# Optimization experiments

Measured on AMD Instinct MI355X. Metric: run time of the kernel, lower is better.

Reference implementation:

```python
import jax, jax.numpy as jnp
import numpy as np

N = 21  # nodes per graph (20 laser sectors + 1 robot node)
MAX_RANGE = 10.0
_bound = np.linspace(-np.pi / 2 - 0.03, np.pi / 2, 21, dtype=np.float32)[:-1]
_angles = _bound + np.float32(np.pi / 20)
ANGLE_FEAT = jnp.asarray(np.stack([np.sin(_angles), np.cos(_angles)], 1), dtype=jnp.float32)  # [20,2]


def _build_nodes(state24):
    # state24: [B,24] -> node features [B,21,7]
    B = state24.shape[0]
    laser = state24[:, :20, None] / MAX_RANGE                       # [B,20,1]
    angle = jnp.broadcast_to(ANGLE_FEAT[None], (B, 20, 2))          # [B,20,2]
    sector = jnp.concatenate([laser, angle, jnp.zeros((B, 20, 4), state24.dtype)], -1)  # [B,20,7]
    robot = jnp.concatenate([jnp.zeros((B, 1, 3), state24.dtype), state24[:, None, 20:]], -1)  # [B,1,7]
    return jnp.concatenate([sector, robot], axis=1)                 # [B,21,7]


def _gatv2(x, Wl, Wr, att, bias, heads, dim):
    # GATv2 over a fully-connected graph with self-loops (dense all-pairs).
    # e_ij = att . leaky_relu(Wl x_j + Wr x_i); alpha = softmax_j; out_i = sum_j alpha_ij (Wl x_j)
    B = x.shape[0]
    gl = (x @ Wl).reshape(B, N, heads, dim)  # source transform [B,j,H,D]
    gr = (x @ Wr).reshape(B, N, heads, dim)  # target transform [B,i,H,D]
    s = jax.nn.leaky_relu(gl[:, None] + gr[:, :, None], negative_slope=0.2)  # [B,i,j,H,D]
    e = jnp.einsum('bijhd,hd->bijh', s, att)                                  # [B,i,j,H]
    alpha = jax.nn.softmax(e, axis=2)                                          # softmax over sources j
    out = jnp.einsum('bijh,bjhd->bihd', alpha, gl).reshape(B, N, heads * dim)
    return out + bias


def setup_inputs() -> dict:
    key = jax.random.key(0)
    ks = jax.random.split(key, 16)
    r = lambda k, shape, s: (jax.random.normal(k, shape, dtype=jnp.float32) * s)
    B = 1024
    return {
        'state24': jax.random.normal(ks[0], (B, 24), dtype=jnp.float32),
        'Wl1': r(ks[1], (7, 256), 0.3), 'Wr1': r(ks[2], (7, 256), 0.3),
        'att1': r(ks[3], (4, 64), 0.1), 'b1': r(ks[4], (256,), 0.02),
        'Wl2': r(ks[5], (256, 64), 0.06), 'Wr2': r(ks[6], (256, 64), 0.06),
        'att2': r(ks[7], (1, 64), 0.1), 'b2': r(ks[8], (64,), 0.02),
        'fc1_w': r(ks[9], (64, 256), 0.12), 'fc1_b': r(ks[10], (256,), 0.02),
        'fc2_w': r(ks[11], (256, 256), 0.06), 'fc2_b': r(ks[12], (256,), 0.02),
        'fc3_w': r(ks[13], (256, 2), 0.06), 'fc3_b': r(ks[14], (2,), 0.02),
    }


def reference(state24, Wl1, Wr1, att1, b1, Wl2, Wr2, att2, b2,
              fc1_w, fc1_b, fc2_w, fc2_b, fc3_w, fc3_b):
    x = _build_nodes(state24)                               # [B,21,7]
    h = jax.nn.elu(_gatv2(x, Wl1, Wr1, att1, b1, 4, 64))    # [B,21,256]
    h = _gatv2(h, Wl2, Wr2, att2, b2, 1, 64)                # [B,21,64]
    nfv = jnp.mean(h, axis=1)                               # global_mean_pool -> [B,64]
    h = jax.nn.relu(nfv @ fc1_w + fc1_b)
    h = jax.nn.relu(h @ fc2_w + fc2_b)
    return jnp.tanh(h @ fc3_w + fc3_b)                      # [B,2]
```

## Files before the change

### kernel.cpp

```cpp
#include <hip/hip_runtime.h>
#include <hip/hip_fp16.h>
#include <math.h>

#define PI_D 3.141592653589793

typedef _Float16 h2 __attribute__((ext_vector_type(2)));
typedef _Float16 h4 __attribute__((ext_vector_type(4)));
typedef _Float16 h8 __attribute__((ext_vector_type(8)));
typedef unsigned short us8 __attribute__((ext_vector_type(8)));
typedef __fp16 f16v2 __attribute__((ext_vector_type(2)));
typedef __fp16 f16v8 __attribute__((ext_vector_type(8)));
typedef float f32x4 __attribute__((ext_vector_type(4)));

#define STR1 264
#define STR2H 72

#define SV(v, a, b) __builtin_shufflevector(v, v, a, b)

static __device__ __forceinline__ h2 pack_h2(float a, float b) {
    return __builtin_bit_cast(h2, __builtin_amdgcn_cvt_pkrtz(a, b));
}

static __device__ __forceinline__ float fdot2(h2 a, h2 b, float c) {
    return __builtin_amdgcn_fdot2(__builtin_bit_cast(f16v2, a),
                                  __builtin_bit_cast(f16v2, b), c, false);
}

static __device__ __forceinline__ h8 habs8(h8 x) {
    us8 u = __builtin_bit_cast(us8, x);
    us8 m = {0x7fff, 0x7fff, 0x7fff, 0x7fff, 0x7fff, 0x7fff, 0x7fff, 0x7fff};
    return __builtin_bit_cast(h8, (us8)(u & m));
}

static __device__ __forceinline__ f32x4 mfma16(h8 a, h8 b, f32x4 c) {
    return __builtin_amdgcn_mfma_f32_16x16x32_f16(
        __builtin_bit_cast(f16v8, a), __builtin_bit_cast(f16v8, b), c, 0, 0, 0);
}

__global__ __launch_bounds__(256) void pack_weights_kernel(
    const float* __restrict__ Wl2, const float* __restrict__ Wr2,
    const float* __restrict__ fc1_w, const float* __restrict__ fc2_w,
    h8* __restrict__ ws)
{
    int idx = blockIdx.x * 256 + threadIdx.x;
    if (idx < 4096) {
        const float* W = idx < 2048 ? Wl2 : Wr2;
        int t = idx & 2047;
        int ntile = t >> 9, rem = t & 511;
        int kchunk = rem >> 6, lane = rem & 63;
        int n = ntile * 16 + (lane & 15);
        int k0 = kchunk * 32 + (lane >> 4) * 8;
        h8 o;
        #pragma unroll
        for (int j = 0; j < 8; ++j) o[j] = (_Float16)W[(k0 + j) * 64 + n];
        ws[idx] = o;
    } else if (idx < 6144) {
        int t = idx - 4096;
        int col = t >> 3, kk = t & 7;
        h8 o;
        #pragma unroll
        for (int j = 0; j < 8; ++j) o[j] = (_Float16)fc1_w[(kk * 8 + j) * 256 + col];
        ws[idx] = o;
    } else {
        int t = idx - 6144;
        int col = t >> 5, kk = t & 31;
        h8 o;
        #pragma unroll
        for (int j = 0; j < 8; ++j) o[j] = (_Float16)fc2_w[(kk * 8 + j) * 256 + col];
        ws[idx] = o;
    }
}

__global__ __launch_bounds__(256, 4) void actor_fused_kernel(
    const float* __restrict__ state24,
    const float* __restrict__ Wl1, const float* __restrict__ Wr1,
    const float* __restrict__ att1, const float* __restrict__ b1,
    const float* __restrict__ att2, const float* __restrict__ b2,
    const float* __restrict__ fc1_b, const float* __restrict__ fc2_b,
    const float* __restrict__ fc3_w, const float* __restrict__ fc3_b,
    const h8* __restrict__ wsL, const h8* __restrict__ wsR,
    const h8* __restrict__ wsF1, const h8* __restrict__ wsF2,
    float* __restrict__ out, int B)
{
    const int bix = blockIdx.x;
    if (bix >= B) return;
    const int tid = threadIdx.x;

    __shared__ float sinL[20], cosL[20], laserL[20], robotL[4];
    __shared__ __align__(16) h2 attLh[128];
    __shared__ __align__(16) h2 att2Lh[32];
    __shared__ __align__(16) _Float16 gr1h[21 * STR1];
    __shared__ __align__(16) union {
        struct { _Float16 gl1h[21 * STR1];
                 float ePf[84 * 24];
                 float uv[168]; } p1;
        struct { _Float16 gl2h[21 * STR2H];
                 _Float16 gr2h[21 * STR2H];
                 _Float16 gl2hT[64 * 32];
                 float e2[32 * 24];
                 float u2v2[42];
                 _Float16 nfvh[64]; _Float16 hah[256]; _Float16 hbh[256]; } p2;
    } U;

    if (tid < 20) {
        double step = (PI_D + 0.03) / 20.0;
        float bound = (float)(-PI_D / 2.0 - 0.03 + (double)tid * step);
        float ang = bound + (float)(PI_D / 20.0);
        sinL[tid] = sinf(ang);
        cosL[tid] = cosf(ang);
        laserL[tid] = state24[bix * 24 + tid] * 0.1f;
    }
    if (tid >= 32 && tid < 36) robotL[tid - 32] = state24[bix * 24 + 20 + (tid - 32)];
    if (tid < 128) {
        float2 ap = ((const float2*)att1)[tid];
        attLh[tid] = pack_h2(0.4f * ap.x, 0.4f * ap.y);
    }
    if (tid >= 128 && tid < 160) {
        float2 ap = ((const float2*)att2)[tid - 128];
        att2Lh[tid - 128] = pack_h2(0.4f * ap.x, 0.4f * ap.y);
    }
    __syncthreads();

    {
        const int d2 = tid & 127;
        const int half = tid >> 7;
        float2 wl[7], wr[7];
        #pragma unroll
        for (int k = 0; k < 7; k++) {
            wl[k] = ((const float2*)Wl1)[k * 128 + d2];
            wr[k] = ((const float2*)Wr1)[k * 128 + d2];
        }
        const int base = half * 11;
        #pragma unroll
        for (int nn = 0; nn < 11; ++nn) {
            int node = base + nn;
            if (node < 21) {
                float a0, a1, b0, b1v;
                if (node < 20) {
                    float l = laserL[node], s = sinL[node], c = cosL[node];
                    a0 = l * wl[0].x + s * wl[1].x + c * wl[2].x;
                    a1 = l * wl[0].y + s * wl[1].y + c * wl[2].y;
                    b0 = l * wr[0].x + s * wr[1].x + c * wr[2].x;
                    b1v = l * wr[0].y + s * wr[1].y + c * wr[2].y;
                } else {
                    float r0 = robotL[0], r1 = robotL[1], r2 = robotL[2], r3 = robotL[3];
                    a0 = r0 * wl[3].x + r1 * wl[4].x + r2 * wl[5].x + r3 * wl[6].x;
                    a1 = r0 * wl[3].y + r1 * wl[4].y + r2 * wl[5].y + r3 * wl[6].y;
                    b0 = r0 * wr[3].x + r1 * wr[4].x + r2 * wr[5].x + r3 * wr[6].x;
                    b1v = r0 * wr[3].y + r1 * wr[4].y + r2 * wr[5].y + r3 * wr[6].y;
                }
                ((h2*)(U.p1.gl1h + node * STR1))[d2] = pack_h2(a0, a1);
                ((h2*)(gr1h + node * STR1))[d2] = pack_h2(b0, b1v);
            }
        }
    }
    __syncthreads();

    {
        const int h = tid >> 6;
        const int lane = tid & 63;
        h2 ar[32];
        #pragma unroll
        for (int q = 0; q < 32; ++q) ar[q] = attLh[h * 32 + q];

        if (lane < 63) {
            const int i = lane / 3;
            const int jg = lane - i * 3;
            const h8* gB8 = (const h8*)(gr1h + i * STR1 + h * 64);
            h8 br[8];
            #pragma unroll
            for (int ch = 0; ch < 8; ++ch) br[ch] = gB8[ch];
            const h8* gA8 = (const h8*)(U.p1.gl1h + (jg * 7) * STR1 + h * 64);
            float* eo = U.p1.ePf + (h * 21 + i) * 24 + jg * 7;
            #pragma unroll
            for (int s = 0; s < 7; ++s) {
                float m0 = 0.f, m1 = 0.f;
                #pragma unroll
                for (int ch = 0; ch < 8; ++ch) {
                    h8 x = gA8[ch] + br[ch];
                    h8 ax = habs8(x);
                    m0 = fdot2(SV(ax, 0, 1), ar[ch * 4 + 0], m0);
                    m1 = fdot2(SV(ax, 2, 3), ar[ch * 4 + 1], m1);
                    m0 = fdot2(SV(ax, 4, 5), ar[ch * 4 + 2], m0);
                    m1 = fdot2(SV(ax, 6, 7), ar[ch * 4 + 3], m1);
                }
                eo[s] = m0 + m1;
                gA8 += 33;
            }
        }
        if (tid < 168) {
            int r = tid < 84 ? tid : tid - 84;
            int hu = r / 21, idx = r - hu * 21;
            const _Float16* rowp = (tid < 84 ? U.p1.gl1h : gr1h) + idx * STR1 + hu * 64;
            const h8* row8 = (const h8*)rowp;
            const h2* aru = attLh + hu * 32;
            float l0 = 0.f, l1 = 0.f;
            #pragma unroll
            for (int ch = 0; ch < 8; ++ch) {
                h8 g = row8[ch];
                l0 = fdot2(SV(g, 0, 1), aru[ch * 4 + 0], l0);
                l1 = fdot2(SV(g, 2, 3), aru[ch * 4 + 1], l1);
                l0 = fdot2(SV(g, 4, 5), aru[ch * 4 + 2], l0);
                l1 = fdot2(SV(g, 6, 7), aru[ch * 4 + 3], l1);
            }
            U.p1.uv[tid] = l0 + l1;
        }
    }
    __syncthreads();

    if (tid < 84) {
        int h = tid / 21, i = tid - h * 21;
        float* row = U.p1.ePf + tid * 24;
        const float* uu = U.p1.uv + h * 21;
        float vi = 1.5f * U.p1.uv[84 + h * 21 + i];
        float ebuf[21];
        float m = -1e30f;
        #pragma unroll
        for (int j = 0; j < 21; j++) {
            float e = row[j] + 1.5f * uu[j] + vi;
            ebuf[j] = e;
            m = fmaxf(m, e);
        }
        float s = 0.f;
        #pragma unroll
        for (int j = 0; j < 21; j++) { float v = __expf(ebuf[j] - m); ebuf[j] = v; s += v; }
        float rinv = 1.f / s;
        h8* hp8 = (h8*)(U.p1.ePf) + tid * 6;
        h8 o0, o1, o2;
        #pragma unroll
        for (int q = 0; q < 8; ++q) o0[q] = (_Float16)(ebuf[q] * rinv);
        #pragma unroll
        for (int q = 0; q < 8; ++q) o1[q] = (_Float16)(ebuf[8 + q] * rinv);
        #pragma unroll
        for (int q = 0; q < 5; ++q) o2[q] = (_Float16)(ebuf[16 + q] * rinv);
        o2[5] = (_Float16)0.f; o2[6] = (_Float16)0.f; o2[7] = (_Float16)0.f;
        h8 zz = {};
        hp8[0] = o0; hp8[1] = o1; hp8[2] = o2;
        hp8[3] = zz; hp8[4] = zz; hp8[5] = zz;
    }
    __syncthreads();

    h8 pbL[8], pbR[8];
    {
        const int lane = tid & 63;
        const int w = tid >> 6;
        const h8* bLp = wsL + w * 512 + lane;
        const h8* bRp = wsR + w * 512 + lane;
        #pragma unroll
        for (int kc = 0; kc < 8; ++kc) { pbL[kc] = bLp[kc * 64]; pbR[kc] = bRp[kc * 64]; }

        const int h = w;
        const int mcol = lane & 15;
        const int quad = lane >> 4;
        const h8* Af = (const h8*)U.p1.ePf;
        h8 A0 = Af[(h * 21 + mcol) * 6 + quad];
        int m1r = 16 + mcol; if (m1r > 20) m1r = 20;
        h8 A1 = Af[(h * 21 + m1r) * 6 + quad];
        int rowoff[8];
        #pragma unroll
        for (int jj = 0; jj < 8; ++jj) {
            int rr = quad * 8 + jj;
            rowoff[jj] = (rr > 20 ? 20 : rr) * STR1;
        }
        const int colbase = h * 64 + mcol;
        f32x4 z4 = {0.f, 0.f, 0.f, 0.f};
        #pragma unroll
        for (int t = 0; t < 4; ++t) {
            int col = colbase + t * 16;
            h8 bv;
            #pragma unroll
            for (int jj = 0; jj < 8; ++jj) bv[jj] = U.p1.gl1h[rowoff[jj] + col];
            f32x4 d0 = mfma16(A0, bv, z4);
            f32x4 d1 = mfma16(A1, bv, z4);
            float bb = b1[col];
            #pragma unroll
            for (int r = 0; r < 4; ++r) {
                int n0 = quad * 4 + r;
                float v = d0[r] + bb;
                v = v > 0.f ? v : __expf(v) - 1.f;
                gr1h[n0 * STR1 + col] = (_Float16)v;
                int n1 = 16 + quad * 4 + r;
                if (n1 < 21) {
                    float w2 = d1[r] + bb;
                    w2 = w2 > 0.f ? w2 : __expf(w2) - 1.f;
                    gr1h[n1 * STR1 + col] = (_Float16)w2;
                }
            }
        }
    }
    __syncthreads();

    {
        const int lane = tid & 63;
        const int w = tid >> 6;
        const int mrow = lane & 15;
        const int quad = lane >> 4;
        int rowA1 = 16 + mrow; if (rowA1 > 20) rowA1 = 20;
        const h8* hA0 = (const h8*)(gr1h + mrow * STR1 + quad * 8);
        const h8* hA1 = (const h8*)(gr1h + rowA1 * STR1 + quad * 8);
        f32x4 aL0 = {0.f, 0.f, 0.f, 0.f}, aL1 = {0.f, 0.f, 0.f, 0.f};
        f32x4 aR0 = {0.f, 0.f, 0.f, 0.f}, aR1 = {0.f, 0.f, 0.f, 0.f};
        #pragma unroll
        for (int kc = 0; kc < 8; ++kc) {
            h8 A0 = hA0[kc * 4];
            h8 A1 = hA1[kc * 4];
            aL0 = mfma16(A0, pbL[kc], aL0);
            aL1 = mfma16(A1, pbL[kc], aL1);
            aR0 = mfma16(A0, pbR[kc], aR0);
            aR1 = mfma16(A1, pbR[kc], aR1);
        }
        const int col = w * 16 + mrow;
        #pragma unroll
        for (int r = 0; r < 4; ++r) {
            int row0 = quad * 4 + r;
            U.p2.gl2h[row0 * STR2H + col] = (_Float16)aL0[r];
            U.p2.gr2h[row0 * STR2H + col] = (_Float16)aR0[r];
            int row1 = 16 + row0;
            if (row1 < 21) {
                U.p2.gl2h[row1 * STR2H + col] = (_Float16)aL1[r];
                U.p2.gr2h[row1 * STR2H + col] = (_Float16)aR1[r];
            }
        }
        {
            h2 lo0 = pack_h2(aL0[0], aL0[1]);
            h2 hi0 = pack_h2(aL0[2], aL0[3]);
            h4 p0 = __builtin_shufflevector(lo0, hi0, 0, 1, 2, 3);
            *(h4*)(U.p2.gl2hT + col * 32 + quad * 4) = p0;
            h2 lo1 = pack_h2(aL1[0], aL1[1]);
            h2 hi1 = pack_h2(aL1[2], aL1[3]);
            h4 p1 = __builtin_shufflevector(lo1, hi1, 0, 1, 2, 3);
            *(h4*)(U.p2.gl2hT + col * 32 + 16 + quad * 4) = p1;
        }
    }
    __syncthreads();

    {
        h2 ar2[32];
        #pragma unroll
        for (int q = 0; q < 32; ++q) ar2[q] = att2Lh[q];

        #pragma unroll
        for (int it = 0; it < 2; ++it) {
            int t = it * 256 + tid;
            if (t < 441) {
                int i = t / 21;
                int j = t - i * 21;
                const h8* gA8 = (const h8*)(U.p2.gl2h + j * STR2H);
                const h8* gB8 = (const h8*)(U.p2.gr2h + i * STR2H);
                float m0 = 0.f, m1 = 0.f;
                #pragma unroll
                for (int ch = 0; ch < 8; ++ch) {
                    h8 x = gA8[ch] + gB8[ch];
                    h8 ax = habs8(x);
                    m0 = fdot2(SV(ax, 0, 1), ar2[ch * 4 + 0], m0);
                    m1 = fdot2(SV(ax, 2, 3), ar2[ch * 4 + 1], m1);
                    m0 = fdot2(SV(ax, 4, 5), ar2[ch * 4 + 2], m0);
                    m1 = fdot2(SV(ax, 6, 7), ar2[ch * 4 + 3], m1);
                }
                U.p2.e2[i * 24 + j] = m0 + m1;
            } else if (t < 483) {
                int u = t - 441;
                int r = u < 21 ? u : u - 21;
                const _Float16* rowp = (u < 21 ? U.p2.gl2h : U.p2.gr2h) + r * STR2H;
                const h8* row8 = (const h8*)rowp;
                float l0 = 0.f, l1 = 0.f;
                #pragma unroll
                for (int ch = 0; ch < 8; ++ch) {
                    h8 g = row8[ch];
                    l0 = fdot2(SV(g, 0, 1), ar2[ch * 4 + 0], l0);
                    l1 = fdot2(SV(g, 2, 3), ar2[ch * 4 + 1], l1);
                    l0 = fdot2(SV(g, 4, 5), ar2[ch * 4 + 2], l0);
                    l1 = fdot2(SV(g, 6, 7), ar2[ch * 4 + 3], l1);
                }
                U.p2.u2v2[u] = l0 + l1;
            }
        }
    }
    __syncthreads();

    if (tid < 21) {
        float* row = U.p2.e2 + tid * 24;
        const float* uu = U.p2.u2v2;
        float vi = 1.5f * U.p2.u2v2[21 + tid];
        float ebuf[21];
        float m = -1e30f;
        #pragma unroll
        for (int j = 0; j < 21; j++) {
            float e = row[j] + 1.5f * uu[j] + vi;
            ebuf[j] = e;
            m = fmaxf(m, e);
        }
        float s = 0.f;
        #pragma unroll
        for (int j = 0; j < 21; j++) { float v = __expf(ebuf[j] - m); ebuf[j] = v; s += v; }
        float rinv = 1.f / s;
        h8* hp8 = (h8*)(U.p2.e2) + tid * 6;
        h8 o0, o1, o2;
        #pragma unroll
        for (int q = 0; q < 8; ++q) o0[q] = (_Float16)(ebuf[q] * rinv);
        #pragma unroll
        for (int q = 0; q < 8; ++q) o1[q] = (_Float16)(ebuf[8 + q] * rinv);
        #pragma unroll
        for (int q = 0; q < 5; ++q) o2[q] = (_Float16)(ebuf[16 + q] * rinv);
        o2[5] = (_Float16)0.f; o2[6] = (_Float16)0.f; o2[7] = (_Float16)0.f;
        h8 zz = {};
        hp8[0] = o0; hp8[1] = o1; hp8[2] = o2;
        hp8[3] = zz; hp8[4] = zz; hp8[5] = zz;
    } else if (tid < 87) {
        int z = tid - 21;
        int rr = z / 6, slot = z - rr * 6;
        h8 zz = {};
        ((h8*)U.p2.e2)[(21 + rr) * 6 + slot] = zz;
    }
    __syncthreads();

    {
        const int lane = tid & 63;
        const int w = tid >> 6;
        const int mcol = lane & 15;
        const int quad = lane >> 4;
        const h8* Af2 = (const h8*)U.p2.e2;
        h8 A0 = Af2[mcol * 6 + quad];
        h8 A1 = Af2[(16 + mcol) * 6 + quad];
        h8 bv = *(const h8*)(U.p2.gl2hT + (w * 16 + mcol) * 32 + quad * 8);
        f32x4 z4 = {0.f, 0.f, 0.f, 0.f};
        f32x4 d0 = mfma16(A0, bv, z4);
        f32x4 d1 = mfma16(A1, bv, z4);
        float s = (d0[0] + d0[1]) + (d0[2] + d0[3])
                + (d1[0] + d1[1]) + (d1[2] + d1[3]);
        s += __shfl_xor(s, 16, 64);
        s += __shfl_xor(s, 32, 64);
        if (quad == 0) {
            int col = w * 16 + mcol;
            U.p2.nfvh[col] = (_Float16)(s * (1.f / 21.f) + b2[col]);
        }
    }
    __syncthreads();

    {
        const h8* nf8 = (const h8*)U.p2.nfvh;
        h8 xv[8];
        #pragma unroll
        for (int q = 0; q < 8; ++q) xv[q] = nf8[q];
        const h8* wp = wsF1 + tid * 8;
        float a0 = 0.f, a1 = 0.f, a2 = 0.f, a3 = 0.f;
        #pragma unroll
        for (int kk = 0; kk < 8; ++kk) {
            h8 w = wp[kk];
            h8 xa = xv[kk];
            a0 = fdot2(SV(w, 0, 1), SV(xa, 0, 1), a0);
            a1 = fdot2(SV(w, 2, 3), SV(xa, 2, 3), a1);
            a2 = fdot2(SV(w, 4, 5), SV(xa, 4, 5), a2);
            a3 = fdot2(SV(w, 6, 7), SV(xa, 6, 7), a3);
        }
        float v = (a0 + a1) + (a2 + a3) + fc1_b[tid];
        U.p2.hah[tid] = (_Float16)fmaxf(v, 0.f);
    }
    __syncthreads();

    {
        const h8* ha8 = (const h8*)U.p2.hah;
        const h8* wp = wsF2 + tid * 32;
        float a0 = 0.f, a1 = 0.f, a2 = 0.f, a3 = 0.f;
        #pragma unroll
        for (int q8 = 0; q8 < 32; ++q8) {
            h8 xa = ha8[q8];
            h8 w = wp[q8];
            a0 = fdot2(SV(w, 0, 1), SV(xa, 0, 1), a0);
            a1 = fdot2(SV(w, 2, 3), SV(xa, 2, 3), a1);
            a2 = fdot2(SV(w, 4, 5), SV(xa, 4, 5), a2);
            a3 = fdot2(SV(w, 6, 7), SV(xa, 6, 7), a3);
        }
        float v = (a0 + a1) + (a2 + a3) + fc2_b[tid];
        U.p2.hbh[tid] = (_Float16)fmaxf(v, 0.f);
    }
    __syncthreads();

    if (tid < 128) {
        int o = tid >> 6, l = tid & 63;
        float s = 0.f;
        #pragma unroll
        for (int m = 0; m < 4; m++) {
            int k = l + 64 * m;
            s = fmaf((float)U.p2.hbh[k], fc3_w[k * 2 + o], s);
        }
        #pragma unroll
        for (int off = 32; off >= 1; off >>= 1) s += __shfl_down(s, off, 64);
        if (l == 0) out[bix * 2 + o] = tanhf(s + fc3_b[o]);
    }
}

extern "C" void kernel_launch(void* const* d_in, const int* in_sizes, int n_in,
                              void* d_out, int out_size, void* d_ws, size_t ws_size,
                              hipStream_t stream) {
    const float* state24 = (const float*)d_in[0];
    const float* Wl1 = (const float*)d_in[1];
    const float* Wr1 = (const float*)d_in[2];
    const float* att1 = (const float*)d_in[3];
    const float* b1 = (const float*)d_in[4];
    const float* Wl2 = (const float*)d_in[5];
    const float* Wr2 = (const float*)d_in[6];
    const float* att2 = (const float*)d_in[7];
    const float* b2 = (const float*)d_in[8];
    const float* fc1_w = (const float*)d_in[9];
    const float* fc1_b = (const float*)d_in[10];
    const float* fc2_w = (const float*)d_in[11];
    const float* fc2_b = (const float*)d_in[12];
    const float* fc3_w = (const float*)d_in[13];
    const float* fc3_b = (const float*)d_in[14];
    float* out = (float*)d_out;

    h8* ws = (h8*)d_ws;
    const h8* wsL = ws;
    const h8* wsR = ws + 2048;
    const h8* wsF1 = ws + 4096;
    const h8* wsF2 = ws + 6144;

    pack_weights_kernel<<<56, 256, 0, stream>>>(Wl2, Wr2, fc1_w, fc2_w, ws);

    int B = in_sizes[0] / 24;
    actor_fused_kernel<<<B, 256, 0, stream>>>(
        state24, Wl1, Wr1, att1, b1, att2, b2,
        fc1_b, fc2_b, fc3_w, fc3_b,
        wsL, wsR, wsF1, wsF2, out, B);
}
```

Measured before the change: 127.1 us.

## Coalesce FC weight layout, flatten attention pair loop, pad softmax rows to 32

New measurement: 126.9 us. Within noise of the previous version (-0.1%).

```diff
diff --git a/kernel.cpp b/kernel.cpp
--- a/kernel.cpp
+++ b/kernel.cpp
@@ -56,14 +56,14 @@
         ws[idx] = o;
     } else if (idx < 6144) {
         int t = idx - 4096;
-        int col = t >> 3, kk = t & 7;
+        int kk = t >> 8, col = t & 255;
         h8 o;
         #pragma unroll
         for (int j = 0; j < 8; ++j) o[j] = (_Float16)fc1_w[(kk * 8 + j) * 256 + col];
         ws[idx] = o;
     } else {
         int t = idx - 6144;
-        int col = t >> 5, kk = t & 31;
+        int kk = t >> 8, col = t & 255;
         h8 o;
         #pragma unroll
         for (int j = 0; j < 8; ++j) o[j] = (_Float16)fc2_w[(kk * 8 + j) * 256 + col];
@@ -89,10 +89,10 @@
     __shared__ float sinL[20], cosL[20], laserL[20], robotL[4];
     __shared__ __align__(16) h2 attLh[128];
     __shared__ __align__(16) h2 att2Lh[32];
-    __shared__ __align__(16) _Float16 gr1h[21 * STR1];
+    __shared__ __align__(16) _Float16 gr1h[22 * STR1];
     __shared__ __align__(16) union {
-        struct { _Float16 gl1h[21 * STR1];
-                 float ePf[84 * 24];
+        struct { _Float16 gl1h[22 * STR1];
+                 float ePf[128 * 24];
                  float uv[168]; } p1;
         struct { _Float16 gl2h[21 * STR2H];
                  _Float16 gr2h[21 * STR2H];
@@ -122,6 +122,9 @@
     __syncthreads();
 
     {
+        h8 zz = {};
+        if (tid < 33) ((h8*)U.p1.gl1h)[21 * 33 + tid] = zz;
+
         const int d2 = tid & 127;
         const int half = tid >> 7;
         float2 wl[7], wr[7];
@@ -163,29 +166,24 @@
         #pragma unroll
         for (int q = 0; q < 32; ++q) ar[q] = attLh[h * 32 + q];
 
-        if (lane < 63) {
-            const int i = lane / 3;
-            const int jg = lane - i * 3;
-            const h8* gB8 = (const h8*)(gr1h + i * STR1 + h * 64);
-            h8 br[8];
-            #pragma unroll
-            for (int ch = 0; ch < 8; ++ch) br[ch] = gB8[ch];
-            const h8* gA8 = (const h8*)(U.p1.gl1h + (jg * 7) * STR1 + h * 64);
-            float* eo = U.p1.ePf + (h * 21 + i) * 24 + jg * 7;
-            #pragma unroll
-            for (int s = 0; s < 7; ++s) {
+        for (int it = 0; it < 7; ++it) {
+            int q = it * 64 + lane;
+            if (q < 441) {
+                int i = q / 21;
+                int j = q - i * 21;
+                const h8* gA8 = (const h8*)(U.p1.gl1h + j * STR1 + h * 64);
+                const h8* gB8 = (const h8*)(gr1h + i * STR1 + h * 64);
                 float m0 = 0.f, m1 = 0.f;
                 #pragma unroll
                 for (int ch = 0; ch < 8; ++ch) {
-                    h8 x = gA8[ch] + br[ch];
+                    h8 x = gA8[ch] + gB8[ch];
                     h8 ax = habs8(x);
                     m0 = fdot2(SV(ax, 0, 1), ar[ch * 4 + 0], m0);
                     m1 = fdot2(SV(ax, 2, 3), ar[ch * 4 + 1], m1);
                     m0 = fdot2(SV(ax, 4, 5), ar[ch * 4 + 2], m0);
                     m1 = fdot2(SV(ax, 6, 7), ar[ch * 4 + 3], m1);
                 }
-                eo[s] = m0 + m1;
-                gA8 += 33;
+                U.p1.ePf[(h * 32 + i) * 24 + j] = m0 + m1;
             }
         }
         if (tid < 168) {
@@ -210,7 +208,8 @@
 
     if (tid < 84) {
         int h = tid / 21, i = tid - h * 21;
-        float* row = U.p1.ePf + tid * 24;
+        int r = h * 32 + i;
+        float* row = U.p1.ePf + r * 24;
         const float* uu = U.p1.uv + h * 21;
         float vi = 1.5f * U.p1.uv[84 + h * 21 + i];
         float ebuf[21];
@@ -225,7 +224,7 @@
         #pragma unroll
         for (int j = 0; j < 21; j++) { float v = __expf(ebuf[j] - m); ebuf[j] = v; s += v; }
         float rinv = 1.f / s;
-        h8* hp8 = (h8*)(U.p1.ePf) + tid * 6;
+        h8* hp8 = (h8*)(U.p1.ePf) + r * 6;
         h8 o0, o1, o2;
         #pragma unroll
         for (int q = 0; q < 8; ++q) o0[q] = (_Float16)(ebuf[q] * rinv);
@@ -237,30 +236,32 @@
         h8 zz = {};
         hp8[0] = o0; hp8[1] = o1; hp8[2] = o2;
         hp8[3] = zz; hp8[4] = zz; hp8[5] = zz;
-    }
-    __syncthreads();
-
-    h8 pbL[8], pbR[8];
-    {
+    } else {
+        h8 zz = {};
+        for (int z = tid - 84; z < 264; z += 172) {
+            int rr = z / 6, slot = z - rr * 6;
+            int h = rr / 11, m = 21 + (rr - h * 11);
+            ((h8*)U.p1.ePf)[(h * 32 + m) * 6 + slot] = zz;
+        }
+    }
+    __syncthreads();
+
+    {
+        h8 zz = {};
+        if (tid < 33) ((h8*)gr1h)[21 * 33 + tid] = zz;
+
         const int lane = tid & 63;
-        const int w = tid >> 6;
-        const h8* bLp = wsL + w * 512 + lane;
-        const h8* bRp = wsR + w * 512 + lane;
-        #pragma unroll
-        for (int kc = 0; kc < 8; ++kc) { pbL[kc] = bLp[kc * 64]; pbR[kc] = bRp[kc * 64]; }
-
-        const int h = w;
+        const int h = tid >> 6;
         const int mcol = lane & 15;
         const int quad = lane >> 4;
         const h8* Af = (const h8*)U.p1.ePf;
-        h8 A0 = Af[(h * 21 + mcol) * 6 + quad];
-        int m1r = 16 + mcol; if (m1r > 20) m1r = 20;
-        h8 A1 = Af[(h * 21 + m1r) * 6 + quad];
+        h8 A0 = Af[(h * 32 + mcol) * 6 + quad];
+        h8 A1 = Af[(h * 32 + 16 + mcol) * 6 + quad];
         int rowoff[8];
         #pragma unroll
         for (int jj = 0; jj < 8; ++jj) {
             int rr = quad * 8 + jj;
-            rowoff[jj] = (rr > 20 ? 20 : rr) * STR1;
+            rowoff[jj] = (rr > 21 ? 21 : rr) * STR1;
         }
         const int colbase = h * 64 + mcol;
         f32x4 z4 = {0.f, 0.f, 0.f, 0.f};
@@ -295,19 +296,23 @@
         const int w = tid >> 6;
         const int mrow = lane & 15;
         const int quad = lane >> 4;
-        int rowA1 = 16 + mrow; if (rowA1 > 20) rowA1 = 20;
+        int rowA1 = 16 + mrow; if (rowA1 > 21) rowA1 = 21;
         const h8* hA0 = (const h8*)(gr1h + mrow * STR1 + quad * 8);
         const h8* hA1 = (const h8*)(gr1h + rowA1 * STR1 + quad * 8);
+        const h8* bL = wsL + w * 512 + lane;
+        const h8* bR = wsR + w * 512 + lane;
         f32x4 aL0 = {0.f, 0.f, 0.f, 0.f}, aL1 = {0.f, 0.f, 0.f, 0.f};
         f32x4 aR0 = {0.f, 0.f, 0.f, 0.f}, aR1 = {0.f, 0.f, 0.f, 0.f};
         #pragma unroll
         for (int kc = 0; kc < 8; ++kc) {
             h8 A0 = hA0[kc * 4];
             h8 A1 = hA1[kc * 4];
-            aL0 = mfma16(A0, pbL[kc], aL0);
-            aL1 = mfma16(A1, pbL[kc], aL1);
-            aR0 = mfma16(A0, pbR[kc], aR0);
-            aR1 = mfma16(A1, pbR[kc], aR1);
+            h8 BL = bL[kc * 64];
+            h8 BR = bR[kc * 64];
+            aL0 = mfma16(A0, BL, aL0);
+            aL1 = mfma16(A1, BL, aL1);
+            aR0 = mfma16(A0, BR, aR0);
+            aR1 = mfma16(A1, BR, aR1);
         }
         const int col = w * 16 + mrow;
         #pragma unroll
@@ -439,15 +444,11 @@
 
     {
         const h8* nf8 = (const h8*)U.p2.nfvh;
-        h8 xv[8];
-        #pragma unroll
-        for (int q = 0; q < 8; ++q) xv[q] = nf8[q];
-        const h8* wp = wsF1 + tid * 8;
         float a0 = 0.f, a1 = 0.f, a2 = 0.f, a3 = 0.f;
         #pragma unroll
         for (int kk = 0; kk < 8; ++kk) {
-            h8 w = wp[kk];
-            h8 xa = xv[kk];
+            h8 w = wsF1[kk * 256 + tid];
+            h8 xa = nf8[kk];
             a0 = fdot2(SV(w, 0, 1), SV(xa, 0, 1), a0);
             a1 = fdot2(SV(w, 2, 3), SV(xa, 2, 3), a1);
             a2 = fdot2(SV(w, 4, 5), SV(xa, 4, 5), a2);
@@ -460,12 +461,11 @@
 
     {
         const h8* ha8 = (const h8*)U.p2.hah;
-        const h8* wp = wsF2 + tid * 32;
         float a0 = 0.f, a1 = 0.f, a2 = 0.f, a3 = 0.f;
-        #pragma unroll
-        for (int q8 = 0; q8 < 32; ++q8) {
-            h8 xa = ha8[q8];
-            h8 w = wp[q8];
+        #pragma unroll 8
+        for (int kk = 0; kk < 32; ++kk) {
+            h8 w = wsF2[kk * 256 + tid];
+            h8 xa = ha8[kk];
             a0 = fdot2(SV(w, 0, 1), SV(xa, 0, 1), a0);
             a1 = fdot2(SV(w, 2, 3), SV(xa, 2, 3), a1);
             a2 = fdot2(SV(w, 4, 5), SV(xa, 4, 5), a2);
```
